# Kernel optimization log

Hardware: AMD Instinct MI355X
Metric: run time of the kernel (lower is better)

The kernel has to match this reference:

```python
import jax, jax.numpy as jnp
import numpy as np

TEMPERATURE = 2.0 / 3.0
LIMIT_A = -0.1
LIMIT_B = 1.1

N_NODES = 50000
N_CLUSTERS = 64
N_RELATIONS = 8
N_EDGES = 1000000


def setup_inputs() -> dict:
    key = jax.random.key(0)
    ks = jax.random.split(key, 6)
    xavier = float(np.sqrt(6.0 / (N_CLUSTERS + N_CLUSTERS)))
    return {
        "assignments": jax.random.normal(ks[0], (N_NODES, N_CLUSTERS), jnp.float32),
        "inter_cluster_logits": jax.random.uniform(ks[1], (N_RELATIONS, N_CLUSTERS, N_CLUSTERS), jnp.float32, -xavier, xavier),
        "log_alpha": jnp.zeros((N_RELATIONS, N_CLUSTERS, N_CLUSTERS), jnp.float32),
        "absent_bias": jnp.zeros((N_RELATIONS,), jnp.float32),
        "edge_index": jax.random.randint(ks[2], (2, N_EDGES), 0, N_NODES, jnp.int32),
        "edge_type": jax.random.randint(ks[3], (N_EDGES,), 0, N_RELATIONS, jnp.int32),
        "neg_edge_index": jax.random.randint(ks[4], (2, N_EDGES), 0, N_NODES, jnp.int32),
        "neg_edge_type": jax.random.randint(ks[5], (N_EDGES,), 0, N_RELATIONS, jnp.int32),
    }


def _edge_logits(assignments, weights, absent_bias, edge_index, edge_type):
    # src, dst: [E, C] gathers (irregular access)
    src = assignments[edge_index[0]]
    dst = assignments[edge_index[1]]
    n_rel = weights.shape[0]
    # torch.bmm(W[et], dst[:, :, None]) == dst @ W[et].T ; compute per relation
    # (fixed small relation loop; avoids materializing [E, C, C]) then select.
    logits_all = jnp.stack(
        [jnp.sum(src * (dst @ weights[r].T), axis=-1) for r in range(n_rel)],
        axis=-1,
    )  # [E, R]
    logits = jnp.take_along_axis(logits_all, edge_type[:, None], axis=1)[:, 0]
    return logits + absent_bias[edge_type]


def reference(assignments, inter_cluster_logits, log_alpha, absent_bias,
              edge_index, edge_type, neg_edge_index, neg_edge_type):
    # Hard-concrete gate, eval mode: z = clamp(sigmoid(log_alpha)*(b-a)+a, 0, 1)
    gate = jnp.clip(jax.nn.sigmoid(log_alpha) * (LIMIT_B - LIMIT_A) + LIMIT_A, 0.0, 1.0)
    weights = jax.nn.sigmoid(inter_cluster_logits) * gate  # [R, C, C]

    pos_logits = _edge_logits(assignments, weights, absent_bias, edge_index, edge_type)
    neg_logits = _edge_logits(assignments, weights, absent_bias, neg_edge_index, neg_edge_type)

    # BCE-with-logits: target=1 -> softplus(-x); target=0 -> softplus(x)
    pos_loss = jnp.mean(jax.nn.softplus(-pos_logits))
    neg_loss = jnp.mean(jax.nn.softplus(neg_logits))
    return pos_loss + neg_loss
```

## Files before the change

kernel.cpp:

```cpp
#include <hip/hip_runtime.h>
#include <hip/hip_bf16.h>
#include <math.h>

#define E_EDGES 1000000
#define N_NODES 50000
#define N_C     64
#define N_REL   8
#define CHB     1024
#define CAP     224
#define NBLK    977

typedef __attribute__((ext_vector_type(4))) float floatx4;
typedef __attribute__((ext_vector_type(2))) float floatx2;

static __device__ __forceinline__ unsigned pk4_fp8(float a, float b, float c, float d) {
    unsigned w = 0;
    w = __builtin_amdgcn_cvt_pk_fp8_f32(a, b, w, false);
    w = __builtin_amdgcn_cvt_pk_fp8_f32(c, d, w, true);
    return w;
}

static __device__ __forceinline__ long long pack64(unsigned lo, unsigned hi) {
    uint2 u; u.x = lo; u.y = hi;
    return __builtin_bit_cast(long long, u);
}

__global__ __launch_bounds__(256) void prep_kernel(
    const float* __restrict__ assign,
    const float* __restrict__ icl,
    const float* __restrict__ la,
    unsigned char* __restrict__ Wp8,
    unsigned char* __restrict__ AS8,
    float* __restrict__ out)
{
    int tid = blockIdx.x * blockDim.x + threadIdx.x;
    int nth = gridDim.x * blockDim.x;
    if (tid == 0) out[0] = 0.0f;

    for (int idx = tid; idx < N_REL * N_C * 16; idx += nth) {
        int row = idx >> 4, dq = idx & 15;
        int q = dq >> 2, c = (dq >> 1) & 1, jh = dq & 1;
        int k0 = (2 * c + jh) * 16 + 4 * q;
        float wv[4];
        #pragma unroll
        for (int b = 0; b < 4; ++b) {
            int srci = (row << 6) + k0 + b;
            float w = 1.0f / (1.0f + __expf(-icl[srci]));
            float g = 1.0f / (1.0f + __expf(-la[srci])) * 1.2f - 0.1f;
            g = fminf(fmaxf(g, 0.0f), 1.0f);
            wv[b] = w * g;
        }
        ((unsigned*)Wp8)[idx] = pk4_fp8(wv[0], wv[1], wv[2], wv[3]);
    }

    for (int n = tid; n < N_NODES; n += nth) {
        const float4* a4 = (const float4*)(assign + (size_t)n * N_C);
        unsigned w[16];
        #pragma unroll
        for (int i = 0; i < 16; ++i) {
            float4 v = a4[i];
            w[i] = pk4_fp8(v.x, v.y, v.z, v.w);
        }
        uint4* as = (uint4*)(AS8 + (size_t)n * N_C);
        #pragma unroll
        for (int q = 0; q < 4; ++q) {
            uint4 o;
            o.x = w[0 * 4 + q];
            o.y = w[1 * 4 + q];
            o.z = w[2 * 4 + q];
            o.w = w[3 * 4 + q];
            as[q] = o;
        }
    }
}

__global__ __launch_bounds__(256, 8) void edge_kernel(
    const unsigned char* __restrict__ AS8,
    const unsigned char* __restrict__ Wp8,
    const float* __restrict__ absent_bias,
    const int* __restrict__ ei, const int* __restrict__ et,
    const int* __restrict__ nei, const int* __restrict__ net,
    float* __restrict__ out)
{
    __shared__ unsigned list[N_REL * CAP];
    __shared__ unsigned cnt[N_REL];
    __shared__ float red[4];
    if (threadIdx.x < N_REL) cnt[threadIdx.x] = 0u;
    __syncthreads();

    int blk = blockIdx.x;
    bool isneg = blk >= NBLK;
    int lb = isneg ? blk - NBLK : blk;
    const int* Es = isneg ? nei : ei;
    const int* Et = isneg ? net : et;
    float sign = isneg ? 1.0f : -1.0f;
    int base = lb * CHB;
    int elim = min(base + CHB, E_EDGES);

    for (int e = base + threadIdx.x; e < elim; e += 256) {
        int s = Es[e];
        int d = Es[E_EDGES + e];
        int r = Et[e];
        unsigned rank = atomicAdd(&cnt[r], 1u);
        if (rank < CAP) list[r * CAP + rank] = (unsigned)s | ((unsigned)d << 16);
    }
    __syncthreads();

    int lane = threadIdx.x & 63;
    int wid  = threadIdx.x >> 6;
    int n16  = lane & 15;
    int quad = lane >> 4;
    float loss = 0.0f;

    for (int r = 0; r < N_REL; ++r) {
        int n_r = min((int)cnt[r], CAP);
        if (n_r == 0) continue;
        float bias = absent_bias[r];
        uint4 wfm[4];
        #pragma unroll
        for (int mt = 0; mt < 4; ++mt)
            wfm[mt] = *(const uint4*)(Wp8 + ((r * 64 + mt * 16 + n16) << 6) + quad * 16);

        for (int g = wid; g * 16 < n_r; g += 4) {
            int idx = g * 16 + n16;
            bool valid = idx < n_r;
            unsigned rec = list[r * CAP + (valid ? idx : 0)];
            int src = rec & 0xFFFF;
            int dst = rec >> 16;
            uint4 S = *(const uint4*)(AS8 + ((size_t)src << 6) + quad * 16);
            uint4 D = *(const uint4*)(AS8 + ((size_t)dst << 6) + quad * 16);
            long long bD0 = pack64(D.x, D.y);
            long long bD1 = pack64(D.z, D.w);
            floatx4 ac[4];
            #pragma unroll
            for (int mt = 0; mt < 4; ++mt) {
                floatx4 z = {0.0f, 0.0f, 0.0f, 0.0f};
                z = __builtin_amdgcn_mfma_f32_16x16x32_fp8_fp8(
                        pack64(wfm[mt].x, wfm[mt].y), bD0, z, 0, 0, 0);
                ac[mt] = __builtin_amdgcn_mfma_f32_16x16x32_fp8_fp8(
                        pack64(wfm[mt].z, wfm[mt].w), bD1, z, 0, 0, 0);
            }
            unsigned sw[4] = {S.x, S.y, S.z, S.w};
            float dot = 0.0f;
            #pragma unroll
            for (int mt = 0; mt < 4; ++mt) {
                floatx2 lo = __builtin_amdgcn_cvt_pk_f32_fp8((int)sw[mt], false);
                floatx2 hi = __builtin_amdgcn_cvt_pk_f32_fp8((int)sw[mt], true);
                dot = fmaf(lo.x, ac[mt][0], dot);
                dot = fmaf(lo.y, ac[mt][1], dot);
                dot = fmaf(hi.x, ac[mt][2], dot);
                dot = fmaf(hi.y, ac[mt][3], dot);
            }
            dot += __shfl_xor(dot, 16);
            dot += __shfl_xor(dot, 32);
            if (quad == 0 && valid) {
                float x = sign * (dot + bias);
                loss += fmaxf(x, 0.0f) + __logf(1.0f + __expf(-fabsf(x)));
            }
        }
    }

    loss += __shfl_xor(loss, 1);
    loss += __shfl_xor(loss, 2);
    loss += __shfl_xor(loss, 4);
    loss += __shfl_xor(loss, 8);
    loss += __shfl_xor(loss, 16);
    loss += __shfl_xor(loss, 32);
    if (lane == 0) red[wid] = loss;
    __syncthreads();
    if (threadIdx.x == 0)
        atomicAdd(out, (red[0] + red[1] + red[2] + red[3]) * (1.0f / (float)E_EDGES));
}

extern "C" void kernel_launch(void* const* d_in, const int* in_sizes, int n_in,
                              void* d_out, int out_size, void* d_ws, size_t ws_size,
                              hipStream_t stream) {
    const float* assign = (const float*)d_in[0];
    const float* icl    = (const float*)d_in[1];
    const float* la     = (const float*)d_in[2];
    const float* ab     = (const float*)d_in[3];
    const int*   ei     = (const int*)d_in[4];
    const int*   et     = (const int*)d_in[5];
    const int*   nei    = (const int*)d_in[6];
    const int*   net    = (const int*)d_in[7];
    float* out = (float*)d_out;

    char* basep = (char*)d_ws;
    unsigned char* Wp8 = (unsigned char*)basep;
    unsigned char* AS8 = (unsigned char*)(basep + 65536);

    prep_kernel<<<256, 256, 0, stream>>>(assign, icl, la, Wp8, AS8, out);
    edge_kernel<<<2 * NBLK, 256, 0, stream>>>(AS8, Wp8, ab, ei, et, nei, net, out);
}
```

Before: 137.3 us.

## Flatten relation groups into one work list and prefetch next group's gathers

Builds a shared list of 16-edge groups across all relations (filled by thread 0), so the four waves share work evenly and no longer wait on a per-relation loop with partial tails. Each wave software-pipelines its loop by issuing the gathers of the next group's source and destination rows before computing the current group. Weight fragments are reloaded from global (cached) memory every group instead of once per relation. The serial list construction by one thread and the extra registers for the prefetched rows are added costs.

Measured after the change: 162.3 us. 1.18x slower.

```diff
diff --git a/kernel.cpp b/kernel.cpp
--- a/kernel.cpp
+++ b/kernel.cpp
@@ -84,6 +84,8 @@
 {
     __shared__ unsigned list[N_REL * CAP];
     __shared__ unsigned cnt[N_REL];
+    __shared__ unsigned glist[128];
+    __shared__ int ng_s;
     __shared__ float red[4];
     if (threadIdx.x < N_REL) cnt[threadIdx.x] = 0u;
     __syncthreads();
@@ -106,58 +108,78 @@
     }
     __syncthreads();
 
+    if (threadIdx.x == 0) {
+        int t = 0;
+        for (int r = 0; r < N_REL; ++r) {
+            int nr = min((int)cnt[r], CAP);
+            for (int b = 0; b < nr; b += 16) {
+                int c = min(16, nr - b);
+                glist[t++] = ((unsigned)r << 16) | ((unsigned)b << 8) | (unsigned)c;
+            }
+        }
+        ng_s = t;
+    }
+    __syncthreads();
+    int ng = ng_s;
+
     int lane = threadIdx.x & 63;
     int wid  = threadIdx.x >> 6;
     int n16  = lane & 15;
     int quad = lane >> 4;
     float loss = 0.0f;
 
-    for (int r = 0; r < N_REL; ++r) {
-        int n_r = min((int)cnt[r], CAP);
-        if (n_r == 0) continue;
-        float bias = absent_bias[r];
-        uint4 wfm[4];
-        #pragma unroll
-        for (int mt = 0; mt < 4; ++mt)
-            wfm[mt] = *(const uint4*)(Wp8 + ((r * 64 + mt * 16 + n16) << 6) + quad * 16);
-
-        for (int g = wid; g * 16 < n_r; g += 4) {
-            int idx = g * 16 + n16;
-            bool valid = idx < n_r;
-            unsigned rec = list[r * CAP + (valid ? idx : 0)];
-            int src = rec & 0xFFFF;
-            int dst = rec >> 16;
-            uint4 S = *(const uint4*)(AS8 + ((size_t)src << 6) + quad * 16);
-            uint4 D = *(const uint4*)(AS8 + ((size_t)dst << 6) + quad * 16);
-            long long bD0 = pack64(D.x, D.y);
-            long long bD1 = pack64(D.z, D.w);
-            floatx4 ac[4];
-            #pragma unroll
-            for (int mt = 0; mt < 4; ++mt) {
-                floatx4 z = {0.0f, 0.0f, 0.0f, 0.0f};
-                z = __builtin_amdgcn_mfma_f32_16x16x32_fp8_fp8(
-                        pack64(wfm[mt].x, wfm[mt].y), bD0, z, 0, 0, 0);
-                ac[mt] = __builtin_amdgcn_mfma_f32_16x16x32_fp8_fp8(
-                        pack64(wfm[mt].z, wfm[mt].w), bD1, z, 0, 0, 0);
-            }
-            unsigned sw[4] = {S.x, S.y, S.z, S.w};
-            float dot = 0.0f;
-            #pragma unroll
-            for (int mt = 0; mt < 4; ++mt) {
-                floatx2 lo = __builtin_amdgcn_cvt_pk_f32_fp8((int)sw[mt], false);
-                floatx2 hi = __builtin_amdgcn_cvt_pk_f32_fp8((int)sw[mt], true);
-                dot = fmaf(lo.x, ac[mt][0], dot);
-                dot = fmaf(lo.y, ac[mt][1], dot);
-                dot = fmaf(hi.x, ac[mt][2], dot);
-                dot = fmaf(hi.y, ac[mt][3], dot);
-            }
-            dot += __shfl_xor(dot, 16);
-            dot += __shfl_xor(dot, 32);
-            if (quad == 0 && valid) {
-                float x = sign * (dot + bias);
-                loss += fmaxf(x, 0.0f) + __logf(1.0f + __expf(-fabsf(x)));
-            }
-        }
+    int gi = wid;
+    unsigned ge = 0;
+    uint4 S = {0, 0, 0, 0}, D = {0, 0, 0, 0};
+    if (gi < ng) {
+        ge = glist[gi];
+        int r = ge >> 16, b = (ge >> 8) & 255, c = ge & 255;
+        unsigned rec = list[r * CAP + b + min(n16, c - 1)];
+        S = *(const uint4*)(AS8 + ((size_t)(rec & 0xFFFF) << 6) + quad * 16);
+        D = *(const uint4*)(AS8 + ((size_t)(rec >> 16) << 6) + quad * 16);
+    }
+    while (gi < ng) {
+        int giN = gi + 4;
+        unsigned geN = 0;
+        uint4 SN = {0, 0, 0, 0}, DN = {0, 0, 0, 0};
+        if (giN < ng) {
+            geN = glist[giN];
+            int rN = geN >> 16, bN = (geN >> 8) & 255, cN = geN & 255;
+            unsigned recN = list[rN * CAP + bN + min(n16, cN - 1)];
+            SN = *(const uint4*)(AS8 + ((size_t)(recN & 0xFFFF) << 6) + quad * 16);
+            DN = *(const uint4*)(AS8 + ((size_t)(recN >> 16) << 6) + quad * 16);
+        }
+
+        int r = ge >> 16, c = ge & 255;
+        long long bD0 = pack64(D.x, D.y);
+        long long bD1 = pack64(D.z, D.w);
+        floatx4 ac[4];
+        #pragma unroll
+        for (int mt = 0; mt < 4; ++mt) {
+            uint4 wf = *(const uint4*)(Wp8 + ((r * 64 + mt * 16 + n16) << 6) + quad * 16);
+            floatx4 z = {0.0f, 0.0f, 0.0f, 0.0f};
+            z = __builtin_amdgcn_mfma_f32_16x16x32_fp8_fp8(pack64(wf.x, wf.y), bD0, z, 0, 0, 0);
+            ac[mt] = __builtin_amdgcn_mfma_f32_16x16x32_fp8_fp8(pack64(wf.z, wf.w), bD1, z, 0, 0, 0);
+        }
+        unsigned sw[4] = {S.x, S.y, S.z, S.w};
+        float dot = 0.0f;
+        #pragma unroll
+        for (int mt = 0; mt < 4; ++mt) {
+            floatx2 lo = __builtin_amdgcn_cvt_pk_f32_fp8((int)sw[mt], false);
+            floatx2 hi = __builtin_amdgcn_cvt_pk_f32_fp8((int)sw[mt], true);
+            dot = fmaf(lo.x, ac[mt][0], dot);
+            dot = fmaf(lo.y, ac[mt][1], dot);
+            dot = fmaf(hi.x, ac[mt][2], dot);
+            dot = fmaf(hi.y, ac[mt][3], dot);
+        }
+        dot += __shfl_xor(dot, 16);
+        dot += __shfl_xor(dot, 32);
+        if (quad == 0 && n16 < c) {
+            float x = sign * (dot + absent_bias[r]);
+            loss += fmaxf(x, 0.0f) + __logf(1.0f + __expf(-fabsf(x)));
+        }
+
+        gi = giN; ge = geN; S = SN; D = DN;
     }
 
     loss += __shfl_xor(loss, 1);
```

## Double-buffer edge gathers, process two groups per iteration, and enlarge per-block chunks

Applied to the files above, without the earlier changes.

The edge loop now handles two 16-edge groups per iteration and prefetches the next pair's source and destination fp8 rows before running the current MFMAs. This is meant to hide gather latency and add instruction-level parallelism. The chunk per block doubles (2048 edges, CAP 384) and the occupancy hint drops from 8 to 4 blocks per CU, which raises register and LDS use per block. Fewer blocks also amortize setup costs, but give coarser load balance.

After: 135.1 us. About the same (-1.6%).

```diff
diff --git a/kernel.cpp b/kernel.cpp
--- a/kernel.cpp
+++ b/kernel.cpp
@@ -6,9 +6,9 @@
 #define N_NODES 50000
 #define N_C     64
 #define N_REL   8
-#define CHB     1024
-#define CAP     224
-#define NBLK    977
+#define CHB     2048
+#define CAP     384
+#define NBLK    489
 
 typedef __attribute__((ext_vector_type(4))) float floatx4;
 typedef __attribute__((ext_vector_type(2))) float floatx2;
@@ -74,7 +74,18 @@
     }
 }
 
-__global__ __launch_bounds__(256, 8) void edge_kernel(
+static __device__ __forceinline__ void ldgrp(
+    const unsigned char* __restrict__ AS8, const unsigned* __restrict__ list_r,
+    int n_r, int g, int n16, int quad, uint4& S, uint4& D, bool& v)
+{
+    int idx = g * 16 + n16;
+    v = idx < n_r;
+    unsigned rec = list_r[min(idx, n_r - 1)];
+    S = *(const uint4*)(AS8 + ((size_t)(rec & 0xFFFF) << 6) + quad * 16);
+    D = *(const uint4*)(AS8 + ((size_t)(rec >> 16) << 6) + quad * 16);
+}
+
+__global__ __launch_bounds__(256, 4) void edge_kernel(
     const unsigned char* __restrict__ AS8,
     const unsigned char* __restrict__ Wp8,
     const float* __restrict__ absent_bias,
@@ -116,47 +127,76 @@
         int n_r = min((int)cnt[r], CAP);
         if (n_r == 0) continue;
         float bias = absent_bias[r];
+        const unsigned* list_r = list + r * CAP;
         uint4 wfm[4];
         #pragma unroll
         for (int mt = 0; mt < 4; ++mt)
             wfm[mt] = *(const uint4*)(Wp8 + ((r * 64 + mt * 16 + n16) << 6) + quad * 16);
 
-        for (int g = wid; g * 16 < n_r; g += 4) {
-            int idx = g * 16 + n16;
-            bool valid = idx < n_r;
-            unsigned rec = list[r * CAP + (valid ? idx : 0)];
-            int src = rec & 0xFFFF;
-            int dst = rec >> 16;
-            uint4 S = *(const uint4*)(AS8 + ((size_t)src << 6) + quad * 16);
-            uint4 D = *(const uint4*)(AS8 + ((size_t)dst << 6) + quad * 16);
-            long long bD0 = pack64(D.x, D.y);
-            long long bD1 = pack64(D.z, D.w);
-            floatx4 ac[4];
+        int g = wid;
+        uint4 Sa, Da, Sb, Db;
+        bool va, vb;
+        ldgrp(AS8, list_r, n_r, g,     n16, quad, Sa, Da, va);
+        ldgrp(AS8, list_r, n_r, g + 4, n16, quad, Sb, Db, vb);
+        while (g * 16 < n_r) {
+            int gn = g + 8;
+            uint4 Sa2, Da2, Sb2, Db2;
+            bool va2, vb2;
+            ldgrp(AS8, list_r, n_r, gn,     n16, quad, Sa2, Da2, va2);
+            ldgrp(AS8, list_r, n_r, gn + 4, n16, quad, Sb2, Db2, vb2);
+
+            long long aD0 = pack64(Da.x, Da.y), aD1 = pack64(Da.z, Da.w);
+            long long bD0 = pack64(Db.x, Db.y), bD1 = pack64(Db.z, Db.w);
+            floatx4 aca[4], acb[4];
             #pragma unroll
             for (int mt = 0; mt < 4; ++mt) {
-                floatx4 z = {0.0f, 0.0f, 0.0f, 0.0f};
-                z = __builtin_amdgcn_mfma_f32_16x16x32_fp8_fp8(
-                        pack64(wfm[mt].x, wfm[mt].y), bD0, z, 0, 0, 0);
-                ac[mt] = __builtin_amdgcn_mfma_f32_16x16x32_fp8_fp8(
-                        pack64(wfm[mt].z, wfm[mt].w), bD1, z, 0, 0, 0);
+                floatx4 za = {0.0f, 0.0f, 0.0f, 0.0f};
+                floatx4 zb = {0.0f, 0.0f, 0.0f, 0.0f};
+                za = __builtin_amdgcn_mfma_f32_16x16x32_fp8_fp8(
+                        pack64(wfm[mt].x, wfm[mt].y), aD0, za, 0, 0, 0);
+                zb = __builtin_amdgcn_mfma_f32_16x16x32_fp8_fp8(
+                        pack64(wfm[mt].x, wfm[mt].y), bD0, zb, 0, 0, 0);
+                aca[mt] = __builtin_amdgcn_mfma_f32_16x16x32_fp8_fp8(
+                        pack64(wfm[mt].z, wfm[mt].w), aD1, za, 0, 0, 0);
+                acb[mt] = __builtin_amdgcn_mfma_f32_16x16x32_fp8_fp8(
+                        pack64(wfm[mt].z, wfm[mt].w), bD1, zb, 0, 0, 0);
             }
-            unsigned sw[4] = {S.x, S.y, S.z, S.w};
-            float dot = 0.0f;
+            unsigned swa[4] = {Sa.x, Sa.y, Sa.z, Sa.w};
+            unsigned swb[4] = {Sb.x, Sb.y, Sb.z, Sb.w};
+            float da = 0.0f, db = 0.0f;
             #pragma unroll
             for (int mt = 0; mt < 4; ++mt) {
-                floatx2 lo = __builtin_amdgcn_cvt_pk_f32_fp8((int)sw[mt], false);
-                floatx2 hi = __builtin_amdgcn_cvt_pk_f32_fp8((int)sw[mt], true);
-                dot = fmaf(lo.x, ac[mt][0], dot);
-                dot = fmaf(lo.y, ac[mt][1], dot);
-                dot = fmaf(hi.x, ac[mt][2], dot);
-                dot = fmaf(hi.y, ac[mt][3], dot);
+                floatx2 loa = __builtin_amdgcn_cvt_pk_f32_fp8((int)swa[mt], false);
+                floatx2 hia = __builtin_amdgcn_cvt_pk_f32_fp8((int)swa[mt], true);
+                floatx2 lob = __builtin_amdgcn_cvt_pk_f32_fp8((int)swb[mt], false);
+                floatx2 hib = __builtin_amdgcn_cvt_pk_f32_fp8((int)swb[mt], true);
+                da = fmaf(loa.x, aca[mt][0], da);
+                db = fmaf(lob.x, acb[mt][0], db);
+                da = fmaf(loa.y, aca[mt][1], da);
+                db = fmaf(lob.y, acb[mt][1], db);
+                da = fmaf(hia.x, aca[mt][2], da);
+                db = fmaf(hib.x, acb[mt][2], db);
+                da = fmaf(hia.y, aca[mt][3], da);
+                db = fmaf(hib.y, acb[mt][3], db);
             }
-            dot += __shfl_xor(dot, 16);
-            dot += __shfl_xor(dot, 32);
-            if (quad == 0 && valid) {
-                float x = sign * (dot + bias);
-                loss += fmaxf(x, 0.0f) + __logf(1.0f + __expf(-fabsf(x)));
+            da += __shfl_xor(da, 16);
+            db += __shfl_xor(db, 16);
+            da += __shfl_xor(da, 32);
+            db += __shfl_xor(db, 32);
+            if (quad == 0) {
+                if (va) {
+                    float x = sign * (da + bias);
+                    loss += fmaxf(x, 0.0f) + __logf(1.0f + __expf(-fabsf(x)));
+                }
+                if (vb) {
+                    float x = sign * (db + bias);
+                    loss += fmaxf(x, 0.0f) + __logf(1.0f + __expf(-fabsf(x)));
+                }
             }
+
+            g = gn;
+            Sa = Sa2; Da = Da2; va = va2;
+            Sb = Sb2; Db = Db2; vb = vb2;
         }
     }
 
```
